# Performance work log

Hardware: AMD Instinct MI355X
Metric: run time of the kernel (lower is better)

Reference implementation:

```python
import jax, jax.numpy as jnp
import numpy as np
import math

B, T, C = 4, 2048, 1024
H, D = 16, 64  # n_head, head_dim; H*D == C

def setup_inputs() -> dict:
    key = jax.random.key(0)
    ks = jax.random.split(key, 8)
    s = 1.0 / math.sqrt(C)
    return {
        "x": jax.random.normal(ks[0], (B, T, C), jnp.float32),
        "W_attn": jax.random.normal(ks[1], (C, 3 * C), jnp.float32) * s,
        "b_attn": jax.random.normal(ks[2], (3 * C,), jnp.float32) * 0.02,
        "W_proj": jax.random.normal(ks[3], (C, C), jnp.float32) * s,
        "b_proj": jax.random.normal(ks[4], (C,), jnp.float32) * 0.02,
        "bQ": jax.random.normal(ks[5], (H, D), jnp.float32) * 0.02,
        "bK": jax.random.normal(ks[6], (H, D), jnp.float32) * 0.02,
        "bV": jax.random.normal(ks[7], (H, D), jnp.float32) * 0.02,
    }

def reference(x, W_attn, b_attn, W_proj, b_proj, bQ, bK, bV):
    Bx, Tx, Cx = x.shape
    qkv = x @ W_attn + b_attn                       # [B,T,3C]
    q, k, v = jnp.split(qkv, 3, axis=-1)
    def heads(t):
        return t.reshape(Bx, Tx, H, D).transpose(0, 2, 1, 3)  # [B,H,T,D]
    q = heads(q) + bQ[None, :, None, :]
    k = heads(k) + bK[None, :, None, :]
    v = heads(v) + bV[None, :, None, :]
    scale = 1.0 / math.sqrt(D)
    scores = jnp.einsum('bhqd,bhkd->bhqk', q, k) * scale      # [B,H,T,T]
    causal = jnp.tril(jnp.ones((Tx, Tx), dtype=bool))
    scores = jnp.where(causal[None, None], scores, -jnp.inf)
    att = jax.nn.softmax(scores, axis=-1)
    y = jnp.einsum('bhqk,bhkd->bhqd', att, v)                 # [B,H,T,D]
    y = y.transpose(0, 2, 1, 3).reshape(Bx, Tx, Cx)
    return y @ W_proj + b_proj
```

## Files before the change

kernel.cpp:

```cpp
#include <hip/hip_runtime.h>
#include <hip/hip_bf16.h>

#define BB 4
#define TT 2048
#define CC 1024
#define HH 16
#define DD 64

typedef __bf16 bf16x8 __attribute__((ext_vector_type(8)));
typedef float f32x4 __attribute__((ext_vector_type(4)));
typedef unsigned int u32x4 __attribute__((ext_vector_type(4)));
typedef unsigned int u32x2 __attribute__((ext_vector_type(2)));
typedef unsigned short u16x8 __attribute__((ext_vector_type(8)));
typedef unsigned short u16x4 __attribute__((ext_vector_type(4)));
typedef unsigned int u32;

__device__ __forceinline__ unsigned short f2bf(float f) {
  u32 u = __builtin_bit_cast(u32, f);
  u += 0x7fff + ((u >> 16) & 1);
  return (unsigned short)(u >> 16);
}

__device__ __forceinline__ bf16x8 lds_load8(const unsigned short* p) {
  u32x4 t = *(const u32x4*)p;
  return __builtin_bit_cast(bf16x8, t);
}

__device__ __forceinline__ void g2l16(const unsigned short* g, unsigned short* l) {
  __builtin_amdgcn_global_load_lds(
      (const __attribute__((address_space(1))) u32*)g,
      (__attribute__((address_space(3))) u32*)l, 16, 0, 0);
}

__global__ __launch_bounds__(256) void prep(
    const float* __restrict__ x, const float* __restrict__ Wa,
    const float* __restrict__ Wp, unsigned short* __restrict__ xb,
    unsigned short* __restrict__ Wta, unsigned short* __restrict__ Wtp)
{
  __shared__ unsigned short T[64 * 68];
  const int tid = threadIdx.x;
  const int bid = blockIdx.x;
  if (bid < 4096) {
    int i = (bid * 256 + tid) * 8;
    f32x4 a = *(const f32x4*)(x + i);
    f32x4 b = *(const f32x4*)(x + i + 4);
    u16x8 o;
    o[0] = f2bf(a[0]); o[1] = f2bf(a[1]); o[2] = f2bf(a[2]); o[3] = f2bf(a[3]);
    o[4] = f2bf(b[0]); o[5] = f2bf(b[1]); o[6] = f2bf(b[2]); o[7] = f2bf(b[3]);
    *(u16x8*)(xb + i) = o;
    return;
  }
  const float* W; unsigned short* Wt; int N, n0, k0;
  if (bid < 4096 + 768) {
    int b2 = bid - 4096;  W = Wa; Wt = Wta; N = 3072;
    n0 = (b2 % 48) * 64;  k0 = (b2 / 48) * 64;
  } else {
    int b2 = bid - 4864;  W = Wp; Wt = Wtp; N = 1024;
    n0 = (b2 % 16) * 64;  k0 = (b2 / 16) * 64;
  }
#pragma unroll
  for (int it = 0; it < 4; ++it) {
    int idx = it * 256 + tid;
    int kk = idx >> 4, nn = (idx & 15) * 4;
    f32x4 v = *(const f32x4*)(W + (size_t)(k0 + kk) * N + n0 + nn);
    u16x4 p;
    p[0] = f2bf(v[0]); p[1] = f2bf(v[1]); p[2] = f2bf(v[2]); p[3] = f2bf(v[3]);
    *(u16x4*)(&T[kk * 68 + nn]) = p;
  }
  __syncthreads();
#pragma unroll
  for (int it = 0; it < 4; ++it) {
    int idx = it * 256 + tid;
    int nn = idx >> 4, kc = (idx & 15) * 4;
    u16x4 o;
    o[0] = T[(kc + 0) * 68 + nn];
    o[1] = T[(kc + 1) * 68 + nn];
    o[2] = T[(kc + 2) * 68 + nn];
    o[3] = T[(kc + 3) * 68 + nn];
    *(u16x4*)(Wt + (size_t)(n0 + nn) * 1024 + k0 + kc) = o;
  }
}

__global__ __launch_bounds__(256) void qkv_gemm(
    const unsigned short* __restrict__ xb, const unsigned short* __restrict__ Wt,
    const float* __restrict__ b_attn, const float* __restrict__ bQ,
    const float* __restrict__ bK, const float* __restrict__ bV,
    unsigned short* __restrict__ Qb, unsigned short* __restrict__ Kb,
    unsigned short* __restrict__ Vb)
{
  __shared__ unsigned short Al[128 * 64];
  __shared__ unsigned short Bl[128 * 64];
  const int tid = threadIdx.x;
  const int w = tid >> 6, lane = tid & 63;
  const int l16 = lane & 15, quad = lane >> 4;
  const int nblk = blockIdx.x % 24, mblk = blockIdx.x / 24;
  const int m0 = mblk * 128, n0 = nblk * 128;
  const int wm = (w & 1) * 64, wn = (w >> 1) * 64;

  const int srow = lane >> 3;
  const int schunk = ((lane & 7) ^ (srow & 7)) * 8;
  const unsigned short* ga = xb + (size_t)(m0 + w * 8 + srow) * 1024 + schunk;
  const unsigned short* gb = Wt + (size_t)(n0 + w * 8 + srow) * 1024 + schunk;
  unsigned short* la = &Al[(w * 8) * 64];
  unsigned short* lb = &Bl[(w * 8) * 64];

  f32x4 acc[4][4] = {};

  for (int kb = 0; kb < 1024; kb += 64) {
    __syncthreads();
#pragma unroll
    for (int i = 0; i < 4; ++i) {
      g2l16(ga + kb + (size_t)i * 32 * 1024, la + i * 32 * 64);
      g2l16(gb + kb + (size_t)i * 32 * 1024, lb + i * 32 * 64);
    }
    __syncthreads();
    bf16x8 af[4][2], bfr[4][2];
#pragma unroll
    for (int mi = 0; mi < 4; ++mi)
#pragma unroll
      for (int dk = 0; dk < 2; ++dk)
        af[mi][dk] = lds_load8(
            &Al[(wm + mi * 16 + l16) * 64 + (((dk * 4 + quad) ^ (l16 & 7)) * 8)]);
#pragma unroll
    for (int ni = 0; ni < 4; ++ni)
#pragma unroll
      for (int dk = 0; dk < 2; ++dk)
        bfr[ni][dk] = lds_load8(
            &Bl[(wn + ni * 16 + l16) * 64 + (((dk * 4 + quad) ^ (l16 & 7)) * 8)]);
#pragma unroll
    for (int mi = 0; mi < 4; ++mi)
#pragma unroll
      for (int ni = 0; ni < 4; ++ni) {
        acc[mi][ni] = __builtin_amdgcn_mfma_f32_16x16x32_bf16(
            af[mi][0], bfr[ni][0], acc[mi][ni], 0, 0, 0);
        acc[mi][ni] = __builtin_amdgcn_mfma_f32_16x16x32_bf16(
            af[mi][1], bfr[ni][1], acc[mi][ni], 0, 0, 0);
      }
  }

  unsigned short* dst[4];
  float biasv[4], sc[4];
  int st[4];
#pragma unroll
  for (int ni = 0; ni < 4; ++ni) {
    int col = n0 + wn + ni * 16 + l16;
    int sec = col >> 10, cc = col & 1023;
    const float* hb = (sec == 0) ? bQ : (sec == 1 ? bK : bV);
    biasv[ni] = b_attn[col] + hb[cc];
    sc[ni] = (sec == 0) ? 0.125f * 1.44269504f : 1.0f;
    if (sec == 2) {
      dst[ni] = Vb + (size_t)(cc >> 6) * (DD * TT) + (size_t)(cc & 63) * TT;
      st[ni] = 1;
    } else {
      unsigned short* base = (sec == 0) ? Qb : Kb;
      dst[ni] = base + (size_t)(cc >> 6) * (TT * DD) + (cc & 63);
      st[ni] = 64;
    }
  }
#pragma unroll
  for (int mi = 0; mi < 4; ++mi)
#pragma unroll
    for (int r = 0; r < 4; ++r) {
      int m = m0 + wm + mi * 16 + quad * 4 + r;
      int bidx = m >> 11, t = m & 2047;
      size_t co = (size_t)bidx * (HH * TT * DD);
#pragma unroll
      for (int ni = 0; ni < 4; ++ni)
        dst[ni][co + (size_t)t * st[ni]] = f2bf((acc[mi][ni][r] + biasv[ni]) * sc[ni]);
    }
}

__global__ __launch_bounds__(256) void attn_kernel(
    const unsigned short* __restrict__ Qb, const unsigned short* __restrict__ Kb,
    const unsigned short* __restrict__ Vtg, unsigned short* __restrict__ Yb)
{
  __shared__ unsigned short Kl[64 * 64];
  __shared__ unsigned short Vl[64 * 64];
  __shared__ unsigned short Pl[4 * 32 * 72];
  const int tid = threadIdx.x;
  const int w = tid >> 6, lane = tid & 63;
  const int l16 = lane & 15, quad = lane >> 4;
  const int qt = 15 - (blockIdx.x >> 6);
  const int bh = blockIdx.x & 63;
  const int b = bh >> 4, h = bh & 15;
  const int q0 = qt * 128, qw = q0 + w * 32;

  const unsigned short* Qg = Qb + (size_t)bh * TT * DD;
  const unsigned short* Kg = Kb + (size_t)bh * TT * DD;
  const unsigned short* Vg = Vtg + (size_t)bh * DD * TT;

  bf16x8 qf[2][2];
#pragma unroll
  for (int mi = 0; mi < 2; ++mi)
#pragma unroll
    for (int dk = 0; dk < 2; ++dk) {
      u32x4 t = *(const u32x4*)(Qg + (size_t)(qw + mi * 16 + l16) * 64 + dk * 32 + quad * 8);
      qf[mi][dk] = __builtin_bit_cast(bf16x8, t);
    }

  f32x4 accO[2][4] = {};
  f32x4 accL[2] = {};
  u16x8 o16;
#pragma unroll
  for (int j = 0; j < 8; ++j) o16[j] = 0x3F80;
  const bf16x8 onesf = __builtin_bit_cast(bf16x8, o16);

  const int srow = w * 8 + (lane >> 3);
  const int schunk = ((lane & 7) ^ (srow & 7)) * 8;
  const int kkey = 4 * (srow & 15) + (srow >> 4);
  const unsigned short* gk1 = Kg + (size_t)kkey * 64 + schunk;
  const unsigned short* gk2 = Kg + (size_t)(kkey + 2) * 64 + schunk;
  const unsigned short* gv1 = Vg + (size_t)srow * TT + schunk;
  const unsigned short* gv2 = Vg + (size_t)(srow + 32) * TT + schunk;
  unsigned short* klw = &Kl[w * 512];
  unsigned short* vlw = &Vl[w * 512];

  const int kend = q0 + 64;
  for (int k0 = 0; k0 <= kend; k0 += 64) {
    __syncthreads();
    g2l16(gk1 + (size_t)k0 * 64, klw);
    g2l16(gk2 + (size_t)k0 * 64, klw + 2048);
    g2l16(gv1 + k0, vlw);
    g2l16(gv2 + k0, vlw + 2048);
    __syncthreads();
    if (k0 > qw + 31) continue;

    f32x4 accS[2][4] = {};
#pragma unroll
    for (int ni = 0; ni < 4; ++ni)
#pragma unroll
      for (int dk = 0; dk < 2; ++dk) {
        bf16x8 kf = lds_load8(
            &Kl[(ni * 16 + l16) * 64 + (((dk * 4 + quad) ^ (l16 & 7)) * 8)]);
#pragma unroll
        for (int mi = 0; mi < 2; ++mi)
          accS[mi][ni] = __builtin_amdgcn_mfma_f32_16x16x32_bf16(
              qf[mi][dk], kf, accS[mi][ni], 0, 0, 0);
      }

    const bool maskT = (k0 + 63 > qw);
#pragma unroll
    for (int mi = 0; mi < 2; ++mi)
#pragma unroll
      for (int r = 0; r < 4; ++r) {
        int qrow = qw + mi * 16 + quad * 4 + r;
        float s0 = accS[mi][0][r], s1 = accS[mi][1][r];
        float s2 = accS[mi][2][r], s3 = accS[mi][3][r];
        if (maskT) {
          int kb = k0 + 4 * l16;
          if (kb + 0 > qrow) s0 = -3e38f;
          if (kb + 1 > qrow) s1 = -3e38f;
          if (kb + 2 > qrow) s2 = -3e38f;
          if (kb + 3 > qrow) s3 = -3e38f;
        }
        u32 e0 = __builtin_bit_cast(u32, exp2f(s0));
        u32 e1 = __builtin_bit_cast(u32, exp2f(s1));
        u32 e2 = __builtin_bit_cast(u32, exp2f(s2));
        u32 e3 = __builtin_bit_cast(u32, exp2f(s3));
        u32x2 pv;
        pv[0] = __builtin_amdgcn_perm(e1, e0, 0x07060302);
        pv[1] = __builtin_amdgcn_perm(e3, e2, 0x07060302);
        *(u32x2*)(&Pl[(w * 32 + mi * 16 + quad * 4 + r) * 72 + 4 * l16]) = pv;
      }

#pragma unroll
    for (int kc = 0; kc < 2; ++kc) {
      bf16x8 pf[2];
#pragma unroll
      for (int mi = 0; mi < 2; ++mi)
        pf[mi] = lds_load8(&Pl[(w * 32 + mi * 16 + l16) * 72 + kc * 32 + quad * 8]);
#pragma unroll
      for (int dn = 0; dn < 4; ++dn) {
        bf16x8 vf = lds_load8(
            &Vl[(dn * 16 + l16) * 64 + (((kc * 4 + quad) ^ (l16 & 7)) * 8)]);
#pragma unroll
        for (int mi = 0; mi < 2; ++mi)
          accO[mi][dn] = __builtin_amdgcn_mfma_f32_16x16x32_bf16(
              pf[mi], vf, accO[mi][dn], 0, 0, 0);
      }
#pragma unroll
      for (int mi = 0; mi < 2; ++mi)
        accL[mi] = __builtin_amdgcn_mfma_f32_16x16x32_bf16(
            pf[mi], onesf, accL[mi], 0, 0, 0);
    }
  }

#pragma unroll
  for (int mi = 0; mi < 2; ++mi)
#pragma unroll
    for (int r = 0; r < 4; ++r) {
      int q = qw + mi * 16 + quad * 4 + r;
      float inv = 1.0f / accL[mi][r];
      size_t base = ((size_t)b * TT + q) * CC + h * DD;
#pragma unroll
      for (int dn = 0; dn < 4; ++dn)
        Yb[base + dn * 16 + l16] = f2bf(accO[mi][dn][r] * inv);
    }
}

__global__ __launch_bounds__(256) void proj_gemm(
    const unsigned short* __restrict__ Yb, const unsigned short* __restrict__ Wt,
    const float* __restrict__ bp, float* __restrict__ out)
{
  __shared__ unsigned short Al[128 * 64];
  __shared__ unsigned short Bl[128 * 64];
  const int tid = threadIdx.x;
  const int w = tid >> 6, lane = tid & 63;
  const int l16 = lane & 15, quad = lane >> 4;
  const int nblk = blockIdx.x & 7, mblk = blockIdx.x >> 3;
  const int m0 = mblk * 128, n0 = nblk * 128;
  const int wm = (w & 1) * 64, wn = (w >> 1) * 64;

  const int srow = lane >> 3;
  const int schunk = ((lane & 7) ^ (srow & 7)) * 8;
  const unsigned short* ga = Yb + (size_t)(m0 + w * 8 + srow) * 1024 + schunk;
  const unsigned short* gb = Wt + (size_t)(n0 + w * 8 + srow) * 1024 + schunk;
  unsigned short* la = &Al[(w * 8) * 64];
  unsigned short* lb = &Bl[(w * 8) * 64];

  f32x4 acc[4][4] = {};

  for (int kb = 0; kb < 1024; kb += 64) {
    __syncthreads();
#pragma unroll
    for (int i = 0; i < 4; ++i) {
      g2l16(ga + kb + (size_t)i * 32 * 1024, la + i * 32 * 64);
      g2l16(gb + kb + (size_t)i * 32 * 1024, lb + i * 32 * 64);
    }
    __syncthreads();
    bf16x8 af[4][2], bfr[4][2];
#pragma unroll
    for (int mi = 0; mi < 4; ++mi)
#pragma unroll
      for (int dk = 0; dk < 2; ++dk)
        af[mi][dk] = lds_load8(
            &Al[(wm + mi * 16 + l16) * 64 + (((dk * 4 + quad) ^ (l16 & 7)) * 8)]);
#pragma unroll
    for (int ni = 0; ni < 4; ++ni)
#pragma unroll
      for (int dk = 0; dk < 2; ++dk)
        bfr[ni][dk] = lds_load8(
            &Bl[(wn + ni * 16 + l16) * 64 + (((dk * 4 + quad) ^ (l16 & 7)) * 8)]);
#pragma unroll
    for (int mi = 0; mi < 4; ++mi)
#pragma unroll
      for (int ni = 0; ni < 4; ++ni) {
        acc[mi][ni] = __builtin_amdgcn_mfma_f32_16x16x32_bf16(
            af[mi][0], bfr[ni][0], acc[mi][ni], 0, 0, 0);
        acc[mi][ni] = __builtin_amdgcn_mfma_f32_16x16x32_bf16(
            af[mi][1], bfr[ni][1], acc[mi][ni], 0, 0, 0);
      }
  }

#pragma unroll
  for (int mi = 0; mi < 4; ++mi)
#pragma unroll
    for (int r = 0; r < 4; ++r) {
      int m = m0 + wm + mi * 16 + quad * 4 + r;
#pragma unroll
      for (int ni = 0; ni < 4; ++ni) {
        int c = n0 + wn + ni * 16 + l16;
        out[(size_t)m * 1024 + c] = acc[mi][ni][r] + bp[c];
      }
    }
}

extern "C" void kernel_launch(void* const* d_in, const int* in_sizes, int n_in,
                              void* d_out, int out_size, void* d_ws, size_t ws_size,
                              hipStream_t stream) {
  const float* x      = (const float*)d_in[0];
  const float* W_attn = (const float*)d_in[1];
  const float* b_attn = (const float*)d_in[2];
  const float* W_proj = (const float*)d_in[3];
  const float* b_proj = (const float*)d_in[4];
  const float* bQ     = (const float*)d_in[5];
  const float* bK     = (const float*)d_in[6];
  const float* bV     = (const float*)d_in[7];
  float* out = (float*)d_out;

  unsigned short* xb   = (unsigned short*)d_ws;
  unsigned short* Yb   = xb;
  unsigned short* Wt_a = xb + 8388608;
  unsigned short* Wt_p = Wt_a + 3145728;
  unsigned short* Qb   = Wt_p + 1048576;
  unsigned short* Kb   = Qb + 8388608;
  unsigned short* Vb   = Kb + 8388608;

  prep<<<dim3(4096 + 768 + 256), dim3(256), 0, stream>>>(x, W_attn, W_proj,
                                                         xb, Wt_a, Wt_p);
  qkv_gemm<<<dim3(64 * 24), dim3(256), 0, stream>>>(xb, Wt_a, b_attn, bQ, bK, bV,
                                                    Qb, Kb, Vb);
  attn_kernel<<<dim3(16 * 64), dim3(256), 0, stream>>>(Qb, Kb, Vb, Yb);
  proj_gemm<<<dim3(64 * 8), dim3(256), 0, stream>>>(Yb, Wt_p, b_proj, out);
}
```

Before: 281.2 us.

## Rewrite QKV GEMM as 256x256 double-buffered pipelined kernel with 8 waves

The QKV projection GEMM moves from 128x128 tiles with 4 waves and a single LDS buffer to 256x256 tiles with 8 waves and double-buffered LDS. Global-to-LDS loads for later k-tiles are interleaved with MFMA quarter-blocks, using explicit barriers, waitcnt and setprio. A swizzled block index improves L2 reuse. This aims to hide memory latency and raise arithmetic intensity, at the cost of 128KB of LDS, heavier register use, fragile hand scheduling, and only 384 blocks in the grid.

New measurement: 286.1 us. About the same (+1.7%).

```diff
diff --git a/kernel.cpp b/kernel.cpp
--- a/kernel.cpp
+++ b/kernel.cpp
@@ -81,61 +81,104 @@
   }
 }
 
-__global__ __launch_bounds__(256) void qkv_gemm(
+
+#define BAR() __builtin_amdgcn_s_barrier()
+#define WAIT_LGKM0() do { asm volatile("s_waitcnt lgkmcnt(0)" ::: "memory"); \
+                          __builtin_amdgcn_sched_barrier(0); } while (0)
+#define WAIT_VM(n) asm volatile("s_waitcnt vmcnt(" n ")" ::: "memory")
+
+#define STG(arr, g, S_, row0, kb) do { \
+  g2l16((g) + (size_t)(row0) * 1024 + (kb), &arr[S_][((row0) + w8) * 64]); \
+  g2l16((g) + (size_t)((row0) + 64) * 1024 + (kb), &arr[S_][((row0) + 64 + w8) * 64]); \
+} while (0)
+
+#define LDA(S_, dstv, MI0) \
+  _Pragma("unroll") for (int mi_ = 0; mi_ < 4; ++mi_) \
+  _Pragma("unroll") for (int dk_ = 0; dk_ < 2; ++dk_) \
+    dstv[mi_][dk_] = lds_load8(&Al[S_][(wm + ((MI0) + mi_) * 16 + l16) * 64 + \
+                                       (((dk_ * 4 + quad) ^ (l16 & 7)) * 8)]);
+
+#define LDB(S_, dstv, NI0) \
+  _Pragma("unroll") for (int ni_ = 0; ni_ < 2; ++ni_) \
+  _Pragma("unroll") for (int dk_ = 0; dk_ < 2; ++dk_) \
+    dstv[ni_][dk_] = lds_load8(&Bl[S_][(wn + ((NI0) + ni_) * 16 + l16) * 64 + \
+                                       (((dk_ * 4 + quad) ^ (l16 & 7)) * 8)]);
+
+#define MM(AF, BF, MO, NO) \
+  _Pragma("unroll") for (int mi_ = 0; mi_ < 4; ++mi_) \
+  _Pragma("unroll") for (int ni_ = 0; ni_ < 2; ++ni_) { \
+    acc[(MO) + mi_][(NO) + ni_] = __builtin_amdgcn_mfma_f32_16x16x32_bf16( \
+        AF[mi_][0], BF[ni_][0], acc[(MO) + mi_][(NO) + ni_], 0, 0, 0); \
+    acc[(MO) + mi_][(NO) + ni_] = __builtin_amdgcn_mfma_f32_16x16x32_bf16( \
+        AF[mi_][1], BF[ni_][1], acc[(MO) + mi_][(NO) + ni_], 0, 0, 0); \
+  }
+
+#define TILE(T, SS) do { \
+  bf16x8 a03[4][2], a47[4][2], b01[2][2], b23[2][2]; \
+   \
+  LDA(SS, a03, 0); \
+  LDB(SS, b01, 0); \
+  if ((T) + 1 < 16) { STG(Bl, gB, (SS) ^ 1, 128, ((T) + 1) * 64); } \
+  BAR(); WAIT_LGKM0(); \
+  __builtin_amdgcn_s_setprio(1); MM(a03, b01, 0, 0); __builtin_amdgcn_s_setprio(0); \
+  BAR(); \
+   \
+  LDB(SS, b23, 2); \
+  BAR(); WAIT_LGKM0(); \
+  __builtin_amdgcn_s_setprio(1); MM(a03, b23, 0, 2); __builtin_amdgcn_s_setprio(0); \
+  BAR(); \
+   \
+  LDA(SS, a47, 4); \
+  if ((T) + 2 < 16) { STG(Bl, gB, SS, 0, ((T) + 2) * 64); } \
+  BAR(); WAIT_LGKM0(); \
+  __builtin_amdgcn_s_setprio(1); MM(a47, b23, 4, 2); __builtin_amdgcn_s_setprio(0); \
+  BAR(); \
+   \
+  if ((T) + 2 < 16) { STG(Al, gA, SS, 0, ((T) + 2) * 64); \
+                      STG(Al, gA, SS, 128, ((T) + 2) * 64); } \
+  BAR(); \
+  __builtin_amdgcn_s_setprio(1); MM(a47, b01, 4, 0); __builtin_amdgcn_s_setprio(0); \
+  if ((T) < 14) { WAIT_VM("6"); } else { WAIT_VM("0"); } \
+  BAR(); \
+} while (0)
+
+__global__ __launch_bounds__(512, 2) void qkv_gemm(
     const unsigned short* __restrict__ xb, const unsigned short* __restrict__ Wt,
     const float* __restrict__ b_attn, const float* __restrict__ bQ,
     const float* __restrict__ bK, const float* __restrict__ bV,
     unsigned short* __restrict__ Qb, unsigned short* __restrict__ Kb,
     unsigned short* __restrict__ Vb)
 {
-  __shared__ unsigned short Al[128 * 64];
-  __shared__ unsigned short Bl[128 * 64];
+  __shared__ unsigned short Al[2][256 * 64];
+  __shared__ unsigned short Bl[2][256 * 64];
   const int tid = threadIdx.x;
   const int w = tid >> 6, lane = tid & 63;
   const int l16 = lane & 15, quad = lane >> 4;
-  const int nblk = blockIdx.x % 24, mblk = blockIdx.x / 24;
-  const int m0 = mblk * 128, n0 = nblk * 128;
-  const int wm = (w & 1) * 64, wn = (w >> 1) * 64;
-
-  const int srow = lane >> 3;
-  const int schunk = ((lane & 7) ^ (srow & 7)) * 8;
-  const unsigned short* ga = xb + (size_t)(m0 + w * 8 + srow) * 1024 + schunk;
-  const unsigned short* gb = Wt + (size_t)(n0 + w * 8 + srow) * 1024 + schunk;
-  unsigned short* la = &Al[(w * 8) * 64];
-  unsigned short* lb = &Bl[(w * 8) * 64];
-
-  f32x4 acc[4][4] = {};
-
-  for (int kb = 0; kb < 1024; kb += 64) {
-    __syncthreads();
-#pragma unroll
-    for (int i = 0; i < 4; ++i) {
-      g2l16(ga + kb + (size_t)i * 32 * 1024, la + i * 32 * 64);
-      g2l16(gb + kb + (size_t)i * 32 * 1024, lb + i * 32 * 64);
-    }
-    __syncthreads();
-    bf16x8 af[4][2], bfr[4][2];
-#pragma unroll
-    for (int mi = 0; mi < 4; ++mi)
-#pragma unroll
-      for (int dk = 0; dk < 2; ++dk)
-        af[mi][dk] = lds_load8(
-            &Al[(wm + mi * 16 + l16) * 64 + (((dk * 4 + quad) ^ (l16 & 7)) * 8)]);
-#pragma unroll
-    for (int ni = 0; ni < 4; ++ni)
-#pragma unroll
-      for (int dk = 0; dk < 2; ++dk)
-        bfr[ni][dk] = lds_load8(
-            &Bl[(wn + ni * 16 + l16) * 64 + (((dk * 4 + quad) ^ (l16 & 7)) * 8)]);
-#pragma unroll
-    for (int mi = 0; mi < 4; ++mi)
-#pragma unroll
-      for (int ni = 0; ni < 4; ++ni) {
-        acc[mi][ni] = __builtin_amdgcn_mfma_f32_16x16x32_bf16(
-            af[mi][0], bfr[ni][0], acc[mi][ni], 0, 0, 0);
-        acc[mi][ni] = __builtin_amdgcn_mfma_f32_16x16x32_bf16(
-            af[mi][1], bfr[ni][1], acc[mi][ni], 0, 0, 0);
-      }
+  const int w8 = w * 8;
+
+  const int swz = (blockIdx.x & 7) * 48 + (blockIdx.x >> 3);
+  const int mblk = swz / 12, nblk = swz % 12;
+  const int m0 = mblk * 256, n0 = nblk * 256;
+  const int wm = (w >> 2) * 128;
+  const int wn = (w & 3) * 64;
+
+  const int hrow = tid >> 3;
+  const int sw8 = (((tid & 7) ^ (hrow & 7)) * 8);
+  const unsigned short* gA = xb + (size_t)(m0 + hrow) * 1024 + sw8;
+  const unsigned short* gB = Wt + (size_t)(n0 + hrow) * 1024 + sw8;
+
+  f32x4 acc[8][4] = {};
+
+  STG(Al, gA, 0, 0, 0);   STG(Al, gA, 0, 128, 0);
+  STG(Bl, gB, 0, 0, 0);   STG(Bl, gB, 0, 128, 0);
+  STG(Al, gA, 1, 0, 64);  STG(Al, gA, 1, 128, 64);
+  STG(Bl, gB, 1, 0, 64);
+  WAIT_VM("6");
+  BAR();
+
+  for (int t = 0; t < 16; t += 2) {
+    TILE(t, 0);
+    TILE(t + 1, 1);
   }
 
   unsigned short* dst[4];
@@ -158,7 +201,7 @@
     }
   }
 #pragma unroll
-  for (int mi = 0; mi < 4; ++mi)
+  for (int mi = 0; mi < 8; ++mi)
 #pragma unroll
     for (int r = 0; r < 4; ++r) {
       int m = m0 + wm + mi * 16 + quad * 4 + r;
@@ -388,8 +431,8 @@
 
   prep<<<dim3(4096 + 768 + 256), dim3(256), 0, stream>>>(x, W_attn, W_proj,
                                                          xb, Wt_a, Wt_p);
-  qkv_gemm<<<dim3(64 * 24), dim3(256), 0, stream>>>(xb, Wt_a, b_attn, bQ, bK, bV,
-                                                    Qb, Kb, Vb);
+  qkv_gemm<<<dim3(384), dim3(512), 0, stream>>>(xb, Wt_a, b_attn, bQ, bK, bV,
+                                                Qb, Kb, Vb);
   attn_kernel<<<dim3(16 * 64), dim3(256), 0, stream>>>(Qb, Kb, Vb, Yb);
   proj_gemm<<<dim3(64 * 8), dim3(256), 0, stream>>>(Yb, Wt_p, b_proj, out);
 }
```

## Double-buffer LDS in QKV and projection GEMMs and remap blocks per XCD

Applied to the files above, without the earlier changes.

Both GEMM kernels now use two LDS buffers, so the global-to-LDS load for the next K tile is issued before the MFMA work on the current tile, with one barrier per iteration instead of two. The block index is also remapped so that consecutive blocks on the same XCD share M rows, which should improve L2 reuse of the A operand. The trade-off is double the LDS footprint per block (64KB), which may cut occupancy, plus a dependence on the grid size matching the new 8x8 mapping.

Result: no change. 285.7 us (+1.6%).

```diff
diff --git a/kernel.cpp b/kernel.cpp
--- a/kernel.cpp
+++ b/kernel.cpp
@@ -88,12 +88,13 @@
     unsigned short* __restrict__ Qb, unsigned short* __restrict__ Kb,
     unsigned short* __restrict__ Vb)
 {
-  __shared__ unsigned short Al[128 * 64];
-  __shared__ unsigned short Bl[128 * 64];
+  __shared__ unsigned short Al[2][128 * 64];
+  __shared__ unsigned short Bl[2][128 * 64];
   const int tid = threadIdx.x;
   const int w = tid >> 6, lane = tid & 63;
   const int l16 = lane & 15, quad = lane >> 4;
-  const int nblk = blockIdx.x % 24, mblk = blockIdx.x / 24;
+  const int xcd = blockIdx.x & 7, kk = blockIdx.x >> 3;
+  const int mblk = xcd * 8 + (kk & 7), nblk = kk >> 3;
   const int m0 = mblk * 128, n0 = nblk * 128;
   const int wm = (w & 1) * 64, wn = (w >> 1) * 64;
 
@@ -101,32 +102,39 @@
   const int schunk = ((lane & 7) ^ (srow & 7)) * 8;
   const unsigned short* ga = xb + (size_t)(m0 + w * 8 + srow) * 1024 + schunk;
   const unsigned short* gb = Wt + (size_t)(n0 + w * 8 + srow) * 1024 + schunk;
-  unsigned short* la = &Al[(w * 8) * 64];
-  unsigned short* lb = &Bl[(w * 8) * 64];
 
   f32x4 acc[4][4] = {};
 
-  for (int kb = 0; kb < 1024; kb += 64) {
-    __syncthreads();
-#pragma unroll
-    for (int i = 0; i < 4; ++i) {
-      g2l16(ga + kb + (size_t)i * 32 * 1024, la + i * 32 * 64);
-      g2l16(gb + kb + (size_t)i * 32 * 1024, lb + i * 32 * 64);
-    }
-    __syncthreads();
+#pragma unroll
+  for (int i = 0; i < 4; ++i) {
+    g2l16(ga + (size_t)i * 32 * 1024, &Al[0][(w * 8 + i * 32) * 64]);
+    g2l16(gb + (size_t)i * 32 * 1024, &Bl[0][(w * 8 + i * 32) * 64]);
+  }
+  __syncthreads();
+
+  int cur = 0;
+  for (int t = 0; t < 16; ++t) {
+    if (t < 15) {
+      const int kb = (t + 1) * 64;
+#pragma unroll
+      for (int i = 0; i < 4; ++i) {
+        g2l16(ga + kb + (size_t)i * 32 * 1024, &Al[cur ^ 1][(w * 8 + i * 32) * 64]);
+        g2l16(gb + kb + (size_t)i * 32 * 1024, &Bl[cur ^ 1][(w * 8 + i * 32) * 64]);
+      }
+    }
     bf16x8 af[4][2], bfr[4][2];
 #pragma unroll
     for (int mi = 0; mi < 4; ++mi)
 #pragma unroll
       for (int dk = 0; dk < 2; ++dk)
         af[mi][dk] = lds_load8(
-            &Al[(wm + mi * 16 + l16) * 64 + (((dk * 4 + quad) ^ (l16 & 7)) * 8)]);
+            &Al[cur][(wm + mi * 16 + l16) * 64 + (((dk * 4 + quad) ^ (l16 & 7)) * 8)]);
 #pragma unroll
     for (int ni = 0; ni < 4; ++ni)
 #pragma unroll
       for (int dk = 0; dk < 2; ++dk)
         bfr[ni][dk] = lds_load8(
-            &Bl[(wn + ni * 16 + l16) * 64 + (((dk * 4 + quad) ^ (l16 & 7)) * 8)]);
+            &Bl[cur][(wn + ni * 16 + l16) * 64 + (((dk * 4 + quad) ^ (l16 & 7)) * 8)]);
 #pragma unroll
     for (int mi = 0; mi < 4; ++mi)
 #pragma unroll
@@ -136,6 +144,8 @@
         acc[mi][ni] = __builtin_amdgcn_mfma_f32_16x16x32_bf16(
             af[mi][1], bfr[ni][1], acc[mi][ni], 0, 0, 0);
       }
+    __syncthreads();
+    cur ^= 1;
   }
 
   unsigned short* dst[4];
@@ -302,12 +312,13 @@
     const unsigned short* __restrict__ Yb, const unsigned short* __restrict__ Wt,
     const float* __restrict__ bp, float* __restrict__ out)
 {
-  __shared__ unsigned short Al[128 * 64];
-  __shared__ unsigned short Bl[128 * 64];
+  __shared__ unsigned short Al[2][128 * 64];
+  __shared__ unsigned short Bl[2][128 * 64];
   const int tid = threadIdx.x;
   const int w = tid >> 6, lane = tid & 63;
   const int l16 = lane & 15, quad = lane >> 4;
-  const int nblk = blockIdx.x & 7, mblk = blockIdx.x >> 3;
+  const int xcd = blockIdx.x & 7, kk = blockIdx.x >> 3;
+  const int mblk = xcd * 8 + (kk & 7), nblk = kk >> 3;
   const int m0 = mblk * 128, n0 = nblk * 128;
   const int wm = (w & 1) * 64, wn = (w >> 1) * 64;
 
@@ -315,32 +326,39 @@
   const int schunk = ((lane & 7) ^ (srow & 7)) * 8;
   const unsigned short* ga = Yb + (size_t)(m0 + w * 8 + srow) * 1024 + schunk;
   const unsigned short* gb = Wt + (size_t)(n0 + w * 8 + srow) * 1024 + schunk;
-  unsigned short* la = &Al[(w * 8) * 64];
-  unsigned short* lb = &Bl[(w * 8) * 64];
 
   f32x4 acc[4][4] = {};
 
-  for (int kb = 0; kb < 1024; kb += 64) {
-    __syncthreads();
-#pragma unroll
-    for (int i = 0; i < 4; ++i) {
-      g2l16(ga + kb + (size_t)i * 32 * 1024, la + i * 32 * 64);
-      g2l16(gb + kb + (size_t)i * 32 * 1024, lb + i * 32 * 64);
-    }
-    __syncthreads();
+#pragma unroll
+  for (int i = 0; i < 4; ++i) {
+    g2l16(ga + (size_t)i * 32 * 1024, &Al[0][(w * 8 + i * 32) * 64]);
+    g2l16(gb + (size_t)i * 32 * 1024, &Bl[0][(w * 8 + i * 32) * 64]);
+  }
+  __syncthreads();
+
+  int cur = 0;
+  for (int t = 0; t < 16; ++t) {
+    if (t < 15) {
+      const int kb = (t + 1) * 64;
+#pragma unroll
+      for (int i = 0; i < 4; ++i) {
+        g2l16(ga + kb + (size_t)i * 32 * 1024, &Al[cur ^ 1][(w * 8 + i * 32) * 64]);
+        g2l16(gb + kb + (size_t)i * 32 * 1024, &Bl[cur ^ 1][(w * 8 + i * 32) * 64]);
+      }
+    }
     bf16x8 af[4][2], bfr[4][2];
 #pragma unroll
     for (int mi = 0; mi < 4; ++mi)
 #pragma unroll
       for (int dk = 0; dk < 2; ++dk)
         af[mi][dk] = lds_load8(
-            &Al[(wm + mi * 16 + l16) * 64 + (((dk * 4 + quad) ^ (l16 & 7)) * 8)]);
+            &Al[cur][(wm + mi * 16 + l16) * 64 + (((dk * 4 + quad) ^ (l16 & 7)) * 8)]);
 #pragma unroll
     for (int ni = 0; ni < 4; ++ni)
 #pragma unroll
       for (int dk = 0; dk < 2; ++dk)
         bfr[ni][dk] = lds_load8(
-            &Bl[(wn + ni * 16 + l16) * 64 + (((dk * 4 + quad) ^ (l16 & 7)) * 8)]);
+            &Bl[cur][(wn + ni * 16 + l16) * 64 + (((dk * 4 + quad) ^ (l16 & 7)) * 8)]);
 #pragma unroll
     for (int mi = 0; mi < 4; ++mi)
 #pragma unroll
@@ -350,6 +368,8 @@
         acc[mi][ni] = __builtin_amdgcn_mfma_f32_16x16x32_bf16(
             af[mi][1], bfr[ni][1], acc[mi][ni], 0, 0, 0);
       }
+    __syncthreads();
+    cur ^= 1;
   }
 
 #pragma unroll
```

## Double-buffer K/V tiles in attention and remap GEMM blocks per XCD

Applied to the files above, without the earlier changes.

The attention kernel now double-buffers its K/V tiles in LDS. The next tile's global-to-LDS copy is issued before computing on the current one, which drops one of the two barriers per iteration and lets loads overlap MFMA work. s_setprio hints are added around the MFMA sections. Both GEMMs remap blockIdx so that blocks on the same XCD share M rows, aiming for better L2 reuse. In exchange, LDS use for K/V doubles, which may reduce occupancy, and the new block mapping assumes 64 M-blocks, a size the grids must match exactly.

Result: faster. 272.3 us (-3.2%).

```diff
diff --git a/kernel.cpp b/kernel.cpp
--- a/kernel.cpp
+++ b/kernel.cpp
@@ -93,7 +93,8 @@
   const int tid = threadIdx.x;
   const int w = tid >> 6, lane = tid & 63;
   const int l16 = lane & 15, quad = lane >> 4;
-  const int nblk = blockIdx.x % 24, mblk = blockIdx.x / 24;
+  const int xcd = blockIdx.x & 7, kk = blockIdx.x >> 3;
+  const int mblk = xcd * 8 + (kk & 7), nblk = kk >> 3;
   const int m0 = mblk * 128, n0 = nblk * 128;
   const int wm = (w & 1) * 64, wn = (w >> 1) * 64;
 
@@ -174,8 +175,8 @@
     const unsigned short* __restrict__ Qb, const unsigned short* __restrict__ Kb,
     const unsigned short* __restrict__ Vtg, unsigned short* __restrict__ Yb)
 {
-  __shared__ unsigned short Kl[64 * 64];
-  __shared__ unsigned short Vl[64 * 64];
+  __shared__ unsigned short Kl[2 * 4096];
+  __shared__ unsigned short Vl[2 * 4096];
   __shared__ unsigned short Pl[4 * 32 * 72];
   const int tid = threadIdx.x;
   const int w = tid >> 6, lane = tid & 63;
@@ -212,77 +213,92 @@
   const unsigned short* gk2 = Kg + (size_t)(kkey + 2) * 64 + schunk;
   const unsigned short* gv1 = Vg + (size_t)srow * TT + schunk;
   const unsigned short* gv2 = Vg + (size_t)(srow + 32) * TT + schunk;
-  unsigned short* klw = &Kl[w * 512];
-  unsigned short* vlw = &Vl[w * 512];
 
   const int kend = q0 + 64;
+
+  g2l16(gk1, &Kl[w * 512]);
+  g2l16(gk2, &Kl[w * 512 + 2048]);
+  g2l16(gv1, &Vl[w * 512]);
+  g2l16(gv2, &Vl[w * 512 + 2048]);
+  __syncthreads();
+
+  int cur = 0;
   for (int k0 = 0; k0 <= kend; k0 += 64) {
+    const int nxt = (cur ^ 1) * 4096;
+    if (k0 + 64 <= kend) {
+      g2l16(gk1 + (size_t)(k0 + 64) * 64, &Kl[nxt + w * 512]);
+      g2l16(gk2 + (size_t)(k0 + 64) * 64, &Kl[nxt + w * 512 + 2048]);
+      g2l16(gv1 + (k0 + 64), &Vl[nxt + w * 512]);
+      g2l16(gv2 + (k0 + 64), &Vl[nxt + w * 512 + 2048]);
+    }
+    if (k0 <= qw + 31) {
+      const int co = cur * 4096;
+
+      f32x4 accS[2][4] = {};
+      __builtin_amdgcn_s_setprio(1);
+#pragma unroll
+      for (int ni = 0; ni < 4; ++ni)
+#pragma unroll
+        for (int dk = 0; dk < 2; ++dk) {
+          bf16x8 kf = lds_load8(
+              &Kl[co + (ni * 16 + l16) * 64 + (((dk * 4 + quad) ^ (l16 & 7)) * 8)]);
+#pragma unroll
+          for (int mi = 0; mi < 2; ++mi)
+            accS[mi][ni] = __builtin_amdgcn_mfma_f32_16x16x32_bf16(
+                qf[mi][dk], kf, accS[mi][ni], 0, 0, 0);
+        }
+      __builtin_amdgcn_s_setprio(0);
+
+      const bool maskT = (k0 + 63 > qw);
+#pragma unroll
+      for (int mi = 0; mi < 2; ++mi)
+#pragma unroll
+        for (int r = 0; r < 4; ++r) {
+          int qrow = qw + mi * 16 + quad * 4 + r;
+          float s0 = accS[mi][0][r], s1 = accS[mi][1][r];
+          float s2 = accS[mi][2][r], s3 = accS[mi][3][r];
+          if (maskT) {
+            int kb = k0 + 4 * l16;
+            if (kb + 0 > qrow) s0 = -3e38f;
+            if (kb + 1 > qrow) s1 = -3e38f;
+            if (kb + 2 > qrow) s2 = -3e38f;
+            if (kb + 3 > qrow) s3 = -3e38f;
+          }
+          u32 e0 = __builtin_bit_cast(u32, exp2f(s0));
+          u32 e1 = __builtin_bit_cast(u32, exp2f(s1));
+          u32 e2 = __builtin_bit_cast(u32, exp2f(s2));
+          u32 e3 = __builtin_bit_cast(u32, exp2f(s3));
+          u32x2 pv;
+          pv[0] = __builtin_amdgcn_perm(e1, e0, 0x07060302);
+          pv[1] = __builtin_amdgcn_perm(e3, e2, 0x07060302);
+          *(u32x2*)(&Pl[(w * 32 + mi * 16 + quad * 4 + r) * 72 + 4 * l16]) = pv;
+        }
+
+      __builtin_amdgcn_s_setprio(1);
+#pragma unroll
+      for (int kc = 0; kc < 2; ++kc) {
+        bf16x8 pf[2];
+#pragma unroll
+        for (int mi = 0; mi < 2; ++mi)
+          pf[mi] = lds_load8(&Pl[(w * 32 + mi * 16 + l16) * 72 + kc * 32 + quad * 8]);
+#pragma unroll
+        for (int dn = 0; dn < 4; ++dn) {
+          bf16x8 vf = lds_load8(
+              &Vl[co + (dn * 16 + l16) * 64 + (((kc * 4 + quad) ^ (l16 & 7)) * 8)]);
+#pragma unroll
+          for (int mi = 0; mi < 2; ++mi)
+            accO[mi][dn] = __builtin_amdgcn_mfma_f32_16x16x32_bf16(
+                pf[mi], vf, accO[mi][dn], 0, 0, 0);
+        }
+#pragma unroll
+        for (int mi = 0; mi < 2; ++mi)
+          accL[mi] = __builtin_amdgcn_mfma_f32_16x16x32_bf16(
+              pf[mi], onesf, accL[mi], 0, 0, 0);
+      }
+      __builtin_amdgcn_s_setprio(0);
+    }
     __syncthreads();
-    g2l16(gk1 + (size_t)k0 * 64, klw);
-    g2l16(gk2 + (size_t)k0 * 64, klw + 2048);
-    g2l16(gv1 + k0, vlw);
-    g2l16(gv2 + k0, vlw + 2048);
-    __syncthreads();
-    if (k0 > qw + 31) continue;
-
-    f32x4 accS[2][4] = {};
-#pragma unroll
-    for (int ni = 0; ni < 4; ++ni)
-#pragma unroll
-      for (int dk = 0; dk < 2; ++dk) {
-        bf16x8 kf = lds_load8(
-            &Kl[(ni * 16 + l16) * 64 + (((dk * 4 + quad) ^ (l16 & 7)) * 8)]);
-#pragma unroll
-        for (int mi = 0; mi < 2; ++mi)
-          accS[mi][ni] = __builtin_amdgcn_mfma_f32_16x16x32_bf16(
-              qf[mi][dk], kf, accS[mi][ni], 0, 0, 0);
-      }
-
-    const bool maskT = (k0 + 63 > qw);
-#pragma unroll
-    for (int mi = 0; mi < 2; ++mi)
-#pragma unroll
-      for (int r = 0; r < 4; ++r) {
-        int qrow = qw + mi * 16 + quad * 4 + r;
-        float s0 = accS[mi][0][r], s1 = accS[mi][1][r];
-        float s2 = accS[mi][2][r], s3 = accS[mi][3][r];
-        if (maskT) {
-          int kb = k0 + 4 * l16;
-          if (kb + 0 > qrow) s0 = -3e38f;
-          if (kb + 1 > qrow) s1 = -3e38f;
-          if (kb + 2 > qrow) s2 = -3e38f;
-          if (kb + 3 > qrow) s3 = -3e38f;
-        }
-        u32 e0 = __builtin_bit_cast(u32, exp2f(s0));
-        u32 e1 = __builtin_bit_cast(u32, exp2f(s1));
-        u32 e2 = __builtin_bit_cast(u32, exp2f(s2));
-        u32 e3 = __builtin_bit_cast(u32, exp2f(s3));
-        u32x2 pv;
-        pv[0] = __builtin_amdgcn_perm(e1, e0, 0x07060302);
-        pv[1] = __builtin_amdgcn_perm(e3, e2, 0x07060302);
-        *(u32x2*)(&Pl[(w * 32 + mi * 16 + quad * 4 + r) * 72 + 4 * l16]) = pv;
-      }
-
-#pragma unroll
-    for (int kc = 0; kc < 2; ++kc) {
-      bf16x8 pf[2];
-#pragma unroll
-      for (int mi = 0; mi < 2; ++mi)
-        pf[mi] = lds_load8(&Pl[(w * 32 + mi * 16 + l16) * 72 + kc * 32 + quad * 8]);
-#pragma unroll
-      for (int dn = 0; dn < 4; ++dn) {
-        bf16x8 vf = lds_load8(
-            &Vl[(dn * 16 + l16) * 64 + (((kc * 4 + quad) ^ (l16 & 7)) * 8)]);
-#pragma unroll
-        for (int mi = 0; mi < 2; ++mi)
-          accO[mi][dn] = __builtin_amdgcn_mfma_f32_16x16x32_bf16(
-              pf[mi], vf, accO[mi][dn], 0, 0, 0);
-      }
-#pragma unroll
-      for (int mi = 0; mi < 2; ++mi)
-        accL[mi] = __builtin_amdgcn_mfma_f32_16x16x32_bf16(
-            pf[mi], onesf, accL[mi], 0, 0, 0);
-    }
+    cur ^= 1;
   }
 
 #pragma unroll
@@ -307,7 +323,8 @@
   const int tid = threadIdx.x;
   const int w = tid >> 6, lane = tid & 63;
   const int l16 = lane & 15, quad = lane >> 4;
-  const int nblk = blockIdx.x & 7, mblk = blockIdx.x >> 3;
+  const int xcd = blockIdx.x & 7, kk = blockIdx.x >> 3;
+  const int mblk = xcd * 8 + (kk & 7), nblk = kk >> 3;
   const int m0 = mblk * 128, n0 = nblk * 128;
   const int wm = (w & 1) * 64, wn = (w >> 1) * 64;
 
```
